# Kernel optimization log

Measured on AMD Instinct MI355X. Metric: run time of the kernel, lower is better.

Reference implementation:

```python
import jax, jax.numpy as jnp
import numpy as np

NX = 1024
N_HEAD = 16
B = 2
N = 2048


def setup_inputs() -> dict:
    key = jax.random.key(0)
    k1, k2, k3 = jax.random.split(key, 3)
    x = jax.random.normal(k1, (B, N, NX), dtype=jnp.float32)
    # masked_fill mask: True where attention is NOT allowed (above diagonal)
    mask_self_attention = ~jnp.tril(jnp.ones((N, N), dtype=bool))[None, None]
    c_attn_w = jax.random.normal(k2, (NX, 3 * NX), dtype=jnp.float32) * 0.02
    c_attn_b = jnp.zeros((3 * NX,), dtype=jnp.float32)
    c_proj_w = jax.random.normal(k3, (NX, NX), dtype=jnp.float32) * 0.02
    c_proj_b = jnp.zeros((NX,), dtype=jnp.float32)
    return {
        'x': x,
        'c_attn_w': c_attn_w,
        'c_attn_b': c_attn_b,
        'c_proj_w': c_proj_w,
        'c_proj_b': c_proj_b,
        'mask_self_attention': mask_self_attention,
    }


def reference(x, c_attn_w, c_attn_b, c_proj_w, c_proj_b, mask_self_attention):
    hd = NX // N_HEAD  # head dim = 64
    qkv = x @ c_attn_w + c_attn_b                      # [B,N,3*NX]
    q, k, v = jnp.split(qkv, 3, axis=-1)
    # split heads -> [B,H,N,hd]
    q = q.reshape(B, N, N_HEAD, hd).transpose(0, 2, 1, 3)
    v = v.reshape(B, N, N_HEAD, hd).transpose(0, 2, 1, 3)
    k_t = k.reshape(B, N, N_HEAD, hd).transpose(0, 2, 3, 1)  # [B,H,hd,N]
    present = jnp.stack((k_t.transpose(0, 1, 3, 2), v))      # [2,B,H,N,hd]
    w = jnp.einsum('bhqd,bhdk->bhqk', q, k_t)
    w = w / jnp.sqrt(jnp.float32(hd))  # scale=True
    w = jnp.where(mask_self_attention, jnp.float32(-10000.0), w)
    w = jax.nn.softmax(w, axis=-1)
    a = jnp.einsum('bhqk,bhkd->bhqd', w, v)            # [B,H,N,hd]
    a = a.transpose(0, 2, 1, 3).reshape(B, N, NX)      # merge heads
    a = a @ c_proj_w + c_proj_b
    return (a, present)
```

## Files before the change

kernel.cpp:

```cpp
#include <hip/hip_runtime.h>
#include <cstddef>
#include <cstdint>

#define NX_ 1024
#define NH_ 16
#define HD_ 64
#define B_  2
#define N_  2048
#define M_  (B_ * N_)

typedef __attribute__((ext_vector_type(8))) short bf16x8;
typedef __attribute__((ext_vector_type(4))) float f32x4;

__device__ __forceinline__ unsigned short f2bf(float f) {
    union { float f; unsigned u; } v; v.f = f;
    return (unsigned short)((v.u + 0x7FFFu + ((v.u >> 16) & 1u)) >> 16);
}
__device__ __forceinline__ unsigned pk2bf(float a, float b) {
    return (unsigned)f2bf(a) | ((unsigned)f2bf(b) << 16);
}
__device__ __forceinline__ unsigned pkrnd(float a, float b) {
    union { float f; unsigned u; } ua, ub; ua.f = a; ub.f = b;
    return __builtin_amdgcn_perm(ub.u + 0x8000u, ua.u + 0x8000u, 0x07060302u);
}
__device__ __forceinline__ float exp2_hw(float x) {
    float r;
    asm("v_exp_f32 %0, %1" : "=v"(r) : "v"(x));
    return r;
}

__device__ __forceinline__ void gload_lds16(const void* g, void* l) {
    __builtin_amdgcn_global_load_lds(
        (const __attribute__((address_space(1))) unsigned int*)g,
        (__attribute__((address_space(3))) unsigned int*)l, 16, 0, 0);
}

__global__ __launch_bounds__(256)
void pre_pass(const float* __restrict__ x, unsigned short* __restrict__ xb,
              const float* __restrict__ wqkv, unsigned short* __restrict__ wqkv_t,
              const float* __restrict__ wpr, unsigned short* __restrict__ wproj_t)
{
    const int bid = blockIdx.x, t = threadIdx.x;
    if (bid < 2048) {
        const size_t i = ((size_t)bid * 256 + t) * 8;
        const float4 a = *(const float4*)(x + i);
        const float4 b = *(const float4*)(x + i + 4);
        uint4 o;
        o.x = pk2bf(a.x, a.y); o.y = pk2bf(a.z, a.w);
        o.z = pk2bf(b.x, b.y); o.w = pk2bf(b.z, b.w);
        *(uint4*)(xb + i) = o;
        return;
    }
    __shared__ unsigned short tile[32][40];
    const float* W; unsigned short* Wt; int ncols, n0, k0;
    if (bid < 2048 + 3072) {
        const int b2 = bid - 2048;
        W = wqkv; Wt = wqkv_t; ncols = 3072; n0 = (b2 % 96) * 32; k0 = (b2 / 96) * 32;
    } else {
        const int b3 = bid - 5120;
        W = wpr; Wt = wproj_t; ncols = 1024; n0 = (b3 & 31) * 32; k0 = (b3 >> 5) * 32;
    }
    const int r = t >> 3, c4 = (t & 7) * 4;
    const float4 v = *(const float4*)(W + (size_t)(k0 + r) * ncols + n0 + c4);
    tile[r][c4 + 0] = f2bf(v.x); tile[r][c4 + 1] = f2bf(v.y);
    tile[r][c4 + 2] = f2bf(v.z); tile[r][c4 + 3] = f2bf(v.w);
    __syncthreads();
    uint2 o;
    o.x = (unsigned)tile[c4 + 0][r] | ((unsigned)tile[c4 + 1][r] << 16);
    o.y = (unsigned)tile[c4 + 2][r] | ((unsigned)tile[c4 + 3][r] << 16);
    *(uint2*)(Wt + (size_t)(n0 + r) * 1024 + k0 + c4) = o;
}

template<int NOUT, int MODE>
__global__ __launch_bounds__(256, 3)
void gemm_mfma(const unsigned short* __restrict__ Ab, const unsigned short* __restrict__ Wt,
               const float* __restrict__ bias,
               float* __restrict__ o_pk, float* __restrict__ o_pv,
               unsigned short* __restrict__ o_q, unsigned short* __restrict__ o_k,
               unsigned short* __restrict__ o_vt, float* __restrict__ o_f)
{
    __shared__ __align__(16) unsigned short As[2][128 * 32];
    __shared__ __align__(16) unsigned short Bs[2][128 * 32];
    const int t = threadIdx.x, l = t & 63;
    const int g = l >> 4, q15 = l & 15;
    const int w = t >> 6, wm = w >> 1, wn = w & 1;
    const int m0 = blockIdx.y * 128, j0 = blockIdx.x * 128;

    f32x4 acc[4][4];
#pragma unroll
    for (int i = 0; i < 4; i++)
#pragma unroll
        for (int j = 0; j < 4; j++) { acc[i][j][0]=0.f; acc[i][j][1]=0.f; acc[i][j][2]=0.f; acc[i][j][3]=0.f; }

    const int srow[2] = { (w * 2 + 0) * 16 + (l >> 2), (w * 2 + 1) * 16 + (l >> 2) };
    const int kct0 = (l & 3) ^ (srow[0] & 3);
    const int kct1 = (l & 3) ^ (srow[1] & 3);

#define STAGE(BUF, K0)                                                          \
    do {                                                                        \
        gload_lds16(Ab + (size_t)(m0 + srow[0]) * 1024 + (K0) + kct0 * 8,       \
                    &As[BUF][(w * 2 + 0) * 64 * 8]);                            \
        gload_lds16(Ab + (size_t)(m0 + srow[1]) * 1024 + (K0) + kct1 * 8,       \
                    &As[BUF][(w * 2 + 1) * 64 * 8]);                            \
        gload_lds16(Wt + (size_t)(j0 + srow[0]) * 1024 + (K0) + kct0 * 8,       \
                    &Bs[BUF][(w * 2 + 0) * 64 * 8]);                            \
        gload_lds16(Wt + (size_t)(j0 + srow[1]) * 1024 + (K0) + kct1 * 8,       \
                    &Bs[BUF][(w * 2 + 1) * 64 * 8]);                            \
    } while (0)

    STAGE(0, 0);
    __syncthreads();

    for (int k0 = 0; k0 < 1024; k0 += 32) {
        const int buf = (k0 >> 5) & 1;
        if (k0 + 32 < 1024) STAGE(buf ^ 1, k0 + 32);

        bf16x8 af[4], bf[4];
#pragma unroll
        for (int mt = 0; mt < 4; mt++) {
            const int m = wm * 64 + mt * 16 + q15;
            af[mt] = *(const bf16x8*)&As[buf][m * 32 + ((g ^ (m & 3)) & 3) * 8];
        }
#pragma unroll
        for (int nt = 0; nt < 4; nt++) {
            const int n = wn * 64 + nt * 16 + q15;
            bf[nt] = *(const bf16x8*)&Bs[buf][n * 32 + ((g ^ (n & 3)) & 3) * 8];
        }
#pragma unroll
        for (int mt = 0; mt < 4; mt++)
#pragma unroll
            for (int nt = 0; nt < 4; nt++)
                acc[mt][nt] = __builtin_amdgcn_mfma_f32_16x16x32_bf16(af[mt], bf[nt], acc[mt][nt], 0, 0, 0);

        __syncthreads();
    }

#pragma unroll
    for (int nt = 0; nt < 4; nt++) {
        const int ncol = wn * 64 + nt * 16 + q15;
        const int jc = j0 + ncol;
        const float bz = bias[jc];
        const int sec = jc >> 10, jl = jc & 1023, hh = jl >> 6, dd = jl & 63;
#pragma unroll
        for (int mt = 0; mt < 4; mt++) {
#pragma unroll
            for (int r = 0; r < 4; r++) {
                const int m = m0 + wm * 64 + mt * 16 + g * 4 + r;
                const float val = acc[mt][nt][r] + bz;
                if (MODE == 1) {
                    o_f[(size_t)m * NOUT + jc] = val;
                } else {
                    const int bb = m >> 11, nn = m & 2047;
                    const int bhh = bb * NH_ + hh;
                    const size_t idx = ((size_t)bhh * N_ + nn) * HD_ + dd;
                    if (sec == 0)      o_q[idx] = f2bf(val * 0.18033688f);
                    else if (sec == 1) { o_pk[idx] = val; o_k[idx] = f2bf(val); }
                    else               { o_pv[idx] = val;
                                         o_vt[((size_t)bhh * HD_ + dd) * N_ + nn] = f2bf(val); }
                }
            }
        }
    }
#undef STAGE
}

__global__ __launch_bounds__(256, 4)
void attn_mfma(const unsigned short* __restrict__ q_bf,
               const unsigned short* __restrict__ k_bf,
               const unsigned short* __restrict__ v_t,
               unsigned short* __restrict__ a_pre)
{
    __shared__ __align__(16) unsigned short Ks[2][64 * 64];
    __shared__ __align__(16) unsigned short Vt[2][64 * 64];
    __shared__ __align__(16) unsigned short Ps[64 * 64];

    const int t = threadIdx.x, l = t & 63, w = t >> 6;
    const int g = l >> 4, q15 = l & 15;
    const int bh = (int)blockIdx.x & 31;
    const int qt = 31 - ((int)blockIdx.x >> 5);
    const int b = bh >> 4, h = bh & 15;

    const unsigned short* kb  = k_bf + (size_t)bh * N_ * HD_;
    const unsigned short* vtb = v_t  + (size_t)bh * HD_ * N_;

    const int qrow = w * 16 + q15;
    const unsigned short* qp = q_bf + ((size_t)bh * N_ + (size_t)qt * 64 + qrow) * HD_ + g * 8;
    const bf16x8 qf0 = *(const bf16x8*)(qp);
    const bf16x8 qf1 = *(const bf16x8*)(qp + 32);

    const int sr = t >> 2, sc2 = (t & 3) * 2;
    uint4 stgK0, stgK1, stgV0, stgV1;

#define ISSUE(KT)                                                               \
    do {                                                                        \
        const uint4* ksrc = (const uint4*)(kb + ((size_t)((KT) * 64 + sr)) * HD_ + sc2 * 8); \
        stgK0 = ksrc[0]; stgK1 = ksrc[1];                                       \
        const uint4* vsrc = (const uint4*)(vtb + (size_t)sr * N_ + (KT) * 64 + sc2 * 8);     \
        stgV0 = vsrc[0]; stgV1 = vsrc[1];                                       \
    } while (0)

#define COMMIT(BUF)                                                             \
    do {                                                                        \
        unsigned short* kd = &Ks[BUF][sr * 64];                                 \
        *(uint4*)&kd[((sc2 ^ (sr & 7)) & 7) * 8]       = stgK0;                 \
        *(uint4*)&kd[(((sc2 + 1) ^ (sr & 7)) & 7) * 8] = stgK1;                 \
        unsigned short* vd = &Vt[BUF][sr * 64];                                 \
        *(uint4*)&vd[((sc2 ^ (sr & 7)) & 7) * 8]       = stgV0;                 \
        *(uint4*)&vd[(((sc2 + 1) ^ (sr & 7)) & 7) * 8] = stgV1;                 \
    } while (0)

    ISSUE(0); COMMIT(0);
    __syncthreads();

    float l_i = 0.f;
    f32x4 oacc[4];
#pragma unroll
    for (int i = 0; i < 4; i++) { oacc[i][0]=0.f; oacc[i][1]=0.f; oacc[i][2]=0.f; oacc[i][3]=0.f; }

    int cur = 0;
    char* const prow = (char*)Ps + qrow * 128;
    const int psw = (qrow & 7) << 4;

    for (int kt = 0; kt <= qt; kt++) {
        const bool more = (kt < qt);
        if (more) ISSUE(kt + 1);

        f32x4 sacc[4];
#pragma unroll
        for (int i = 0; i < 4; i++) { sacc[i][0]=0.f; sacc[i][1]=0.f; sacc[i][2]=0.f; sacc[i][3]=0.f; }
        __builtin_amdgcn_s_setprio(1);
#pragma unroll
        for (int kt4 = 0; kt4 < 4; kt4++) {
            const int row = kt4 * 16 + q15;
            const bf16x8 kf0 = *(const bf16x8*)&Ks[cur][row * 64 + ((g ^ (row & 7)) & 7) * 8];
            sacc[kt4] = __builtin_amdgcn_mfma_f32_16x16x32_bf16(kf0, qf0, sacc[kt4], 0, 0, 0);
            const bf16x8 kf1 = *(const bf16x8*)&Ks[cur][row * 64 + (((g + 4) ^ (row & 7)) & 7) * 8];
            sacc[kt4] = __builtin_amdgcn_mfma_f32_16x16x32_bf16(kf1, qf1, sacc[kt4], 0, 0, 0);
        }
        __builtin_amdgcn_s_setprio(0);

        float pe[16];
        if (kt == qt) {
#pragma unroll
            for (int kt4 = 0; kt4 < 4; kt4++)
#pragma unroll
                for (int r = 0; r < 4; r++) {
                    const float s = (kt4 * 16 + g * 4 + r > qrow) ? -1.0e30f : sacc[kt4][r];
                    pe[kt4 * 4 + r] = exp2_hw(s);
                }
        } else {
#pragma unroll
            for (int kt4 = 0; kt4 < 4; kt4++)
#pragma unroll
                for (int r = 0; r < 4; r++) pe[kt4 * 4 + r] = exp2_hw(sacc[kt4][r]);
        }
        {
            float s8[8];
#pragma unroll
            for (int i = 0; i < 8; i++) s8[i] = pe[2 * i] + pe[2 * i + 1];
            const float s0 = (s8[0] + s8[1]) + (s8[2] + s8[3]);
            const float s1 = (s8[4] + s8[5]) + (s8[6] + s8[7]);
            l_i += s0 + s1;
        }
#pragma unroll
        for (int kt4 = 0; kt4 < 4; kt4++) {
            uint2 w2;
            w2.x = pkrnd(pe[kt4 * 4 + 0], pe[kt4 * 4 + 1]);
            w2.y = pkrnd(pe[kt4 * 4 + 2], pe[kt4 * 4 + 3]);
            *(uint2*)(prow + ((kt4 * 32 + g * 8) ^ psw)) = w2;
        }

        {
            const bf16x8 pf0 = *(const bf16x8*)(prow + ((g * 16) ^ psw));
            const bf16x8 pf1 = *(const bf16x8*)(prow + (((g + 4) * 16) ^ psw));
            __builtin_amdgcn_s_setprio(1);
#pragma unroll
            for (int dt = 0; dt < 4; dt++) {
                const int vrow = dt * 16 + q15;
                const bf16x8 vf = *(const bf16x8*)&Vt[cur][vrow * 64 + ((g ^ (vrow & 7)) & 7) * 8];
                oacc[dt] = __builtin_amdgcn_mfma_f32_16x16x32_bf16(vf, pf0, oacc[dt], 0, 0, 0);
            }
#pragma unroll
            for (int dt = 0; dt < 4; dt++) {
                const int vrow = dt * 16 + q15;
                const bf16x8 vf = *(const bf16x8*)&Vt[cur][vrow * 64 + (((g + 4) ^ (vrow & 7)) & 7) * 8];
                oacc[dt] = __builtin_amdgcn_mfma_f32_16x16x32_bf16(vf, pf1, oacc[dt], 0, 0, 0);
            }
            __builtin_amdgcn_s_setprio(0);
        }

        if (more) COMMIT(cur ^ 1);
        __syncthreads();
        cur ^= 1;
    }

    float lt = l_i;
    lt += __shfl_xor(lt, 16);
    lt += __shfl_xor(lt, 32);
    const float inv = 1.0f / lt;

    unsigned short* ap2 = a_pre + ((size_t)(b * N_ + qt * 64 + qrow)) * NX_ + h * 64;
#pragma unroll
    for (int dt = 0; dt < 4; dt++) {
#pragma unroll
        for (int j2 = 0; j2 < 2; j2++) {
            const int d = dt * 16 + g * 4 + j2 * 2;
            *(unsigned*)(ap2 + d) = pkrnd(oacc[dt][j2 * 2] * inv, oacc[dt][j2 * 2 + 1] * inv);
        }
    }
#undef ISSUE
#undef COMMIT
}

extern "C" void kernel_launch(void* const* d_in, const int* in_sizes, int n_in,
                              void* d_out, int out_size, void* d_ws, size_t ws_size,
                              hipStream_t stream)
{
    (void)in_sizes; (void)n_in; (void)out_size; (void)ws_size;
    const float* x    = (const float*)d_in[0];
    const float* wqkv = (const float*)d_in[1];
    const float* bqkv = (const float*)d_in[2];
    const float* wpr  = (const float*)d_in[3];
    const float* bpr  = (const float*)d_in[4];

    float* out   = (float*)d_out;
    float* a_out = out;
    float* pk    = out + (size_t)M_ * NX_;
    float* pv    = pk + (size_t)B_ * NH_ * N_ * HD_;

    const size_t SEG = (size_t)M_ * NX_;
    unsigned short* xb      = (unsigned short*)d_ws;
    unsigned short* q_bf    = xb + SEG;
    unsigned short* k_bf    = q_bf + SEG;
    unsigned short* v_t     = k_bf + SEG;
    unsigned short* wqkv_t  = v_t + SEG;
    unsigned short* wproj_t = wqkv_t + (size_t)3 * NX_ * NX_;
    unsigned short* a_pre   = xb;

    pre_pass<<<2048 + 3072 + 1024, 256, 0, stream>>>(x, xb, wqkv, wqkv_t, wpr, wproj_t);

    gemm_mfma<3 * NX_, 0><<<dim3(24, 32), 256, 0, stream>>>(
        xb, wqkv_t, bqkv, pk, pv, q_bf, k_bf, v_t, nullptr);
    attn_mfma<<<dim3(32 * 32), 256, 0, stream>>>(q_bf, k_bf, v_t, a_pre);
    gemm_mfma<NX_, 1><<<dim3(8, 32), 256, 0, stream>>>(
        a_pre, wproj_t, bpr, nullptr, nullptr, nullptr, nullptr, nullptr, a_out);
}
```

Baseline: 199.4 us.

## Enlarge attention tiles to 128 queries, swizzle GEMM blocks, and refine LDS swizzle

The attention kernel now runs 512-thread blocks covering 128 query rows each, so every K/V tile load is shared by eight waves instead of four. Blocks are remapped so that heads are grouped per XCD and long and short causal rows are interleaved. The GEMMs use a 1D grid with an XCD-aware swizzle for better L2 locality, and their LDS XOR swizzle gains an extra term to cut bank conflicts. The trade-off is fewer attention blocks (512) and coarser causal work granularity, which may hurt load balance and occupancy.

Measured after the change: 198.8 us. Within noise of the previous version (-0.3%).

```diff
diff --git a/kernel.cpp b/kernel.cpp
--- a/kernel.cpp
+++ b/kernel.cpp
@@ -71,7 +71,7 @@
     *(uint2*)(Wt + (size_t)(n0 + r) * 1024 + k0 + c4) = o;
 }
 
-template<int NOUT, int MODE>
+template<int NOUT, int MODE, int GX>
 __global__ __launch_bounds__(256, 3)
 void gemm_mfma(const unsigned short* __restrict__ Ab, const unsigned short* __restrict__ Wt,
                const float* __restrict__ bias,
@@ -84,7 +84,10 @@
     const int t = threadIdx.x, l = t & 63;
     const int g = l >> 4, q15 = l & 15;
     const int w = t >> 6, wm = w >> 1, wn = w & 1;
-    const int m0 = blockIdx.y * 128, j0 = blockIdx.x * 128;
+
+    const int nwg = GX * 32;
+    const int swz = ((int)blockIdx.x & 7) * (nwg / 8) + ((int)blockIdx.x >> 3);
+    const int m0 = (swz / GX) * 128, j0 = (swz % GX) * 128;
 
     f32x4 acc[4][4];
 #pragma unroll
@@ -93,8 +96,8 @@
         for (int j = 0; j < 4; j++) { acc[i][j][0]=0.f; acc[i][j][1]=0.f; acc[i][j][2]=0.f; acc[i][j][3]=0.f; }
 
     const int srow[2] = { (w * 2 + 0) * 16 + (l >> 2), (w * 2 + 1) * 16 + (l >> 2) };
-    const int kct0 = (l & 3) ^ (srow[0] & 3);
-    const int kct1 = (l & 3) ^ (srow[1] & 3);
+    const int kct0 = ((l & 3) ^ (srow[0] & 3) ^ ((srow[0] >> 2) & 3)) & 3;
+    const int kct1 = ((l & 3) ^ (srow[1] & 3) ^ ((srow[1] >> 2) & 3)) & 3;
 
 #define STAGE(BUF, K0)                                                          \
     do {                                                                        \
@@ -119,12 +122,12 @@
 #pragma unroll
         for (int mt = 0; mt < 4; mt++) {
             const int m = wm * 64 + mt * 16 + q15;
-            af[mt] = *(const bf16x8*)&As[buf][m * 32 + ((g ^ (m & 3)) & 3) * 8];
+            af[mt] = *(const bf16x8*)&As[buf][m * 32 + ((g ^ (m & 3) ^ ((m >> 2) & 3)) & 3) * 8];
         }
 #pragma unroll
         for (int nt = 0; nt < 4; nt++) {
             const int n = wn * 64 + nt * 16 + q15;
-            bf[nt] = *(const bf16x8*)&Bs[buf][n * 32 + ((g ^ (n & 3)) & 3) * 8];
+            bf[nt] = *(const bf16x8*)&Bs[buf][n * 32 + ((g ^ (n & 3) ^ ((n >> 2) & 3)) & 3) * 8];
         }
 #pragma unroll
         for (int mt = 0; mt < 4; mt++)
@@ -164,7 +167,7 @@
 #undef STAGE
 }
 
-__global__ __launch_bounds__(256, 4)
+__global__ __launch_bounds__(512, 2)
 void attn_mfma(const unsigned short* __restrict__ q_bf,
                const unsigned short* __restrict__ k_bf,
                const unsigned short* __restrict__ v_t,
@@ -172,41 +175,40 @@
 {
     __shared__ __align__(16) unsigned short Ks[2][64 * 64];
     __shared__ __align__(16) unsigned short Vt[2][64 * 64];
-    __shared__ __align__(16) unsigned short Ps[64 * 64];
+    __shared__ __align__(16) unsigned short Ps[128 * 64];
 
     const int t = threadIdx.x, l = t & 63, w = t >> 6;
     const int g = l >> 4, q15 = l & 15;
-    const int bh = (int)blockIdx.x & 31;
-    const int qt = 31 - ((int)blockIdx.x >> 5);
+
+    const int bid = (int)blockIdx.x;
+    const int x = bid & 7, r = bid >> 3;
+    const int bh = x * 4 + (r & 3);
+    const int j = r >> 2;
+    const int qt = (j < 8) ? (15 - j) : (j - 8);
     const int b = bh >> 4, h = bh & 15;
 
     const unsigned short* kb  = k_bf + (size_t)bh * N_ * HD_;
     const unsigned short* vtb = v_t  + (size_t)bh * HD_ * N_;
 
     const int qrow = w * 16 + q15;
-    const unsigned short* qp = q_bf + ((size_t)bh * N_ + (size_t)qt * 64 + qrow) * HD_ + g * 8;
+    const int qg = qt * 128 + qrow;
+    const unsigned short* qp = q_bf + ((size_t)bh * N_ + qg) * HD_ + g * 8;
     const bf16x8 qf0 = *(const bf16x8*)(qp);
     const bf16x8 qf1 = *(const bf16x8*)(qp + 32);
 
-    const int sr = t >> 2, sc2 = (t & 3) * 2;
-    uint4 stgK0, stgK1, stgV0, stgV1;
+    const int sr = t >> 3, s8 = t & 7;
+    uint4 stgK, stgV;
 
 #define ISSUE(KT)                                                               \
     do {                                                                        \
-        const uint4* ksrc = (const uint4*)(kb + ((size_t)((KT) * 64 + sr)) * HD_ + sc2 * 8); \
-        stgK0 = ksrc[0]; stgK1 = ksrc[1];                                       \
-        const uint4* vsrc = (const uint4*)(vtb + (size_t)sr * N_ + (KT) * 64 + sc2 * 8);     \
-        stgV0 = vsrc[0]; stgV1 = vsrc[1];                                       \
+        stgK = *(const uint4*)(kb + ((size_t)((KT) * 64 + sr)) * HD_ + s8 * 8); \
+        stgV = *(const uint4*)(vtb + (size_t)sr * N_ + (KT) * 64 + s8 * 8);     \
     } while (0)
 
 #define COMMIT(BUF)                                                             \
     do {                                                                        \
-        unsigned short* kd = &Ks[BUF][sr * 64];                                 \
-        *(uint4*)&kd[((sc2 ^ (sr & 7)) & 7) * 8]       = stgK0;                 \
-        *(uint4*)&kd[(((sc2 + 1) ^ (sr & 7)) & 7) * 8] = stgK1;                 \
-        unsigned short* vd = &Vt[BUF][sr * 64];                                 \
-        *(uint4*)&vd[((sc2 ^ (sr & 7)) & 7) * 8]       = stgV0;                 \
-        *(uint4*)&vd[(((sc2 + 1) ^ (sr & 7)) & 7) * 8] = stgV1;                 \
+        *(uint4*)&Ks[BUF][sr * 64 + ((s8 ^ (sr & 7)) & 7) * 8] = stgK;          \
+        *(uint4*)&Vt[BUF][sr * 64 + ((s8 ^ (sr & 7)) & 7) * 8] = stgV;          \
     } while (0)
 
     ISSUE(0); COMMIT(0);
@@ -220,9 +222,10 @@
     int cur = 0;
     char* const prow = (char*)Ps + qrow * 128;
     const int psw = (qrow & 7) << 4;
-
-    for (int kt = 0; kt <= qt; kt++) {
-        const bool more = (kt < qt);
+    const int ktmax = 2 * qt + 1;
+
+    for (int kt = 0; kt <= ktmax; kt++) {
+        const bool more = (kt < ktmax);
         if (more) ISSUE(kt + 1);
 
         f32x4 sacc[4];
@@ -240,26 +243,27 @@
         __builtin_amdgcn_s_setprio(0);
 
         float pe[16];
-        if (kt == qt) {
+        if (kt >= 2 * qt) {
 #pragma unroll
             for (int kt4 = 0; kt4 < 4; kt4++)
 #pragma unroll
-                for (int r = 0; r < 4; r++) {
-                    const float s = (kt4 * 16 + g * 4 + r > qrow) ? -1.0e30f : sacc[kt4][r];
-                    pe[kt4 * 4 + r] = exp2_hw(s);
+                for (int rr = 0; rr < 4; rr++) {
+                    const int kcg = kt * 64 + kt4 * 16 + g * 4 + rr;
+                    const float s = (kcg > qg) ? -1.0e30f : sacc[kt4][rr];
+                    pe[kt4 * 4 + rr] = exp2_hw(s);
                 }
         } else {
 #pragma unroll
             for (int kt4 = 0; kt4 < 4; kt4++)
 #pragma unroll
-                for (int r = 0; r < 4; r++) pe[kt4 * 4 + r] = exp2_hw(sacc[kt4][r]);
+                for (int rr = 0; rr < 4; rr++) pe[kt4 * 4 + rr] = exp2_hw(sacc[kt4][rr]);
         }
         {
-            float s8[8];
-#pragma unroll
-            for (int i = 0; i < 8; i++) s8[i] = pe[2 * i] + pe[2 * i + 1];
-            const float s0 = (s8[0] + s8[1]) + (s8[2] + s8[3]);
-            const float s1 = (s8[4] + s8[5]) + (s8[6] + s8[7]);
+            float s8v[8];
+#pragma unroll
+            for (int i = 0; i < 8; i++) s8v[i] = pe[2 * i] + pe[2 * i + 1];
+            const float s0 = (s8v[0] + s8v[1]) + (s8v[2] + s8v[3]);
+            const float s1 = (s8v[4] + s8v[5]) + (s8v[6] + s8v[7]);
             l_i += s0 + s1;
         }
 #pragma unroll
@@ -299,7 +303,7 @@
     lt += __shfl_xor(lt, 32);
     const float inv = 1.0f / lt;
 
-    unsigned short* ap2 = a_pre + ((size_t)(b * N_ + qt * 64 + qrow)) * NX_ + h * 64;
+    unsigned short* ap2 = a_pre + ((size_t)(b * N_ + qg)) * NX_ + h * 64;
 #pragma unroll
     for (int dt = 0; dt < 4; dt++) {
 #pragma unroll
@@ -339,9 +343,9 @@
 
     pre_pass<<<2048 + 3072 + 1024, 256, 0, stream>>>(x, xb, wqkv, wqkv_t, wpr, wproj_t);
 
-    gemm_mfma<3 * NX_, 0><<<dim3(24, 32), 256, 0, stream>>>(
+    gemm_mfma<3 * NX_, 0, 24><<<768, 256, 0, stream>>>(
         xb, wqkv_t, bqkv, pk, pv, q_bf, k_bf, v_t, nullptr);
-    attn_mfma<<<dim3(32 * 32), 256, 0, stream>>>(q_bf, k_bf, v_t, a_pre);
-    gemm_mfma<NX_, 1><<<dim3(8, 32), 256, 0, stream>>>(
+    attn_mfma<<<512, 512, 0, stream>>>(q_bf, k_bf, v_t, a_pre);
+    gemm_mfma<NX_, 1, 8><<<256, 256, 0, stream>>>(
         a_pre, wproj_t, bpr, nullptr, nullptr, nullptr, nullptr, nullptr, a_out);
 }
```
